# Kernel tuning notes

Measured on AMD Instinct MI355X. Metric: run time of the kernel, lower is better.

The kernel has to match this reference:

```python
import jax, jax.numpy as jnp
import numpy as np

N = 40000      # nodes
E = 400000     # edges
G = 64         # graphs in batch
IN = 128       # input feature dim
D = 64         # num_hidden (per-head out dim)
H = 4          # heads per layer
C = 10         # num_classes
SLOPE = 0.2    # leaky_relu negative slope


def setup_inputs() -> dict:
    key = jax.random.key(0)
    ks = jax.random.split(key, 16)

    def p(k, shape, fan):
        return jax.random.normal(k, shape, jnp.float32) * (1.0 / np.sqrt(fan))

    x = jax.random.normal(ks[0], (N, IN), jnp.float32)
    src = jax.random.randint(ks[1], (E,), 0, N, dtype=jnp.int32)
    dst = jax.random.randint(ks[2], (E,), 0, N, dtype=jnp.int32)
    graph_id = jnp.sort(jax.random.randint(ks[3], (N,), 0, G, dtype=jnp.int32))

    W0 = p(ks[4], (IN, H * D), IN)
    al0 = p(ks[5], (H, D), D)
    ar0 = p(ks[6], (H, D), D)
    W1 = p(ks[7], (H * D, H * D), H * D)
    al1 = p(ks[8], (H, D), D)
    ar1 = p(ks[9], (H, D), D)
    W2 = p(ks[10], (H * D, H * D), H * D)
    al2 = p(ks[11], (H, D), D)
    ar2 = p(ks[12], (H, D), D)
    Wc = p(ks[13], (D, C), D)
    bc = jnp.zeros((C,), jnp.float32)
    return dict(x=x, src=src, dst=dst, graph_id=graph_id,
                W0=W0, al0=al0, ar0=ar0, W1=W1, al1=al1, ar1=ar1,
                W2=W2, al2=al2, ar2=ar2, Wc=Wc, bc=bc)


def gat_layer(h, W, al, ar, src, dst, residual, activate):
    # DGL GATConv (no bias): project, per-edge attention, edge-softmax, aggregate.
    n = h.shape[0]
    Hh, Dd = al.shape
    feat = (h @ W).reshape(n, Hh, Dd)                       # [N,H,D]
    el = jnp.einsum('nhd,hd->nh', feat, al)                 # [N,H]
    er = jnp.einsum('nhd,hd->nh', feat, ar)                 # [N,H]
    e = jax.nn.leaky_relu(el[src] + er[dst], SLOPE)         # [E,H]
    # numerically stable edge softmax over incoming edges of each dst node
    m = jax.ops.segment_max(e, dst, num_segments=n)
    m = jnp.where(jnp.isfinite(m), m, 0.0)                  # isolated nodes -> -inf
    ee = jnp.exp(e - m[dst])                                # [E,H]
    denom = jax.ops.segment_sum(ee, dst, num_segments=n)
    alpha = ee / jnp.maximum(denom[dst], 1e-9)              # [E,H]
    msg = feat[src] * alpha[..., None]                      # [E,H,D]
    out = jax.ops.segment_sum(msg, dst, num_segments=n)     # [N,H,D]
    if residual:  # identity residual (in == H*D)
        out = out + h.reshape(n, Hh, Dd)
    if activate:
        out = jax.nn.elu(out)
    return out


def reference(x, src, dst, graph_id, W0, al0, ar0, W1, al1, ar1,
              W2, al2, ar2, Wc, bc):
    h = gat_layer(x, W0, al0, ar0, src, dst, False, True).reshape(N, H * D)
    h = gat_layer(h, W1, al1, ar1, src, dst, True, True).reshape(N, H * D)
    h = gat_layer(h, W2, al2, ar2, src, dst, True, False).mean(axis=1)  # [N,D]
    # mean_nodes readout over batched graphs
    cnt = jax.ops.segment_sum(jnp.ones((N,), jnp.float32), graph_id, num_segments=G)
    hg = jax.ops.segment_sum(h, graph_id, num_segments=G) / jnp.maximum(cnt, 1.0)[:, None]
    return hg @ Wc + bc                                     # [G,C]
```

## Files before the change

kernel.cpp:

```cpp
#include <hip/hip_runtime.h>
#include <hip/hip_bf16.h>
#include <math.h>

#define N_NODES 40000
#define N_EDGES 400000
#define N_GRAPH 64
#define IN_DIM 128
#define HD 256
#define NCLS 10
#define SLOPE 0.2f

typedef __hip_bfloat16 bf16;
typedef __attribute__((ext_vector_type(8))) short short8;
typedef __attribute__((ext_vector_type(4))) float floatx4;

__device__ __forceinline__ float b2f(bf16 x){ return __bfloat162float(x); }
__device__ __forceinline__ bf16  f2b(float x){ return __float2bfloat16(x); }

__device__ __forceinline__ floatx4 unpack4(uint2 u){
  floatx4 f;
  f[0] = __uint_as_float(u.x << 16);
  f[1] = __uint_as_float(u.x & 0xffff0000u);
  f[2] = __uint_as_float(u.y << 16);
  f[3] = __uint_as_float(u.y & 0xffff0000u);
  return f;
}

__device__ __forceinline__ int wave_incl_scan(int x, int lane){
  #pragma unroll
  for (int m=1;m<64;m<<=1){
    int v = __shfl_up(x, m);
    if (lane >= m) x += v;
  }
  return x;
}

__global__ __launch_bounds__(256) void prep_kernel(const float* __restrict__ W0, ushort* __restrict__ Wt0,
                                                   const float* __restrict__ W1, ushort* __restrict__ Wt1,
                                                   const float* __restrict__ W2, ushort* __restrict__ Wt2,
                                                   int* __restrict__ cnt, float* __restrict__ gacc)
{
  int b = blockIdx.x, t = threadIdx.x;
  if (b < 640){
    const float* W; ushort* Wt; int e0, n_el;
    if (b < 128){ W = W0; Wt = Wt0; e0 = b*256; n_el = IN_DIM*HD; }
    else if (b < 384){ W = W1; Wt = Wt1; e0 = (b-128)*256; n_el = HD*HD; }
    else { W = W2; Wt = Wt2; e0 = (b-384)*256; n_el = HD*HD; }
    int e = e0 + t;
    if (e < n_el){
      int k = e >> 8, n = e & 255;
      int idx = (((k>>6)*256 + n)<<6) + (k & 63);
      Wt[idx] = __bfloat16_as_ushort(f2b(W[e]));
    }
  } else if (b < 797){
    int i = (b-640)*256 + t;
    if (i < N_NODES) cnt[i] = 0;
  } else {
    #pragma unroll
    for (int k=0;k<16;++k) gacc[t*16 + k] = 0.f;
  }
}

__global__ __launch_bounds__(256) void hist_kernel(const int* __restrict__ dst, int* __restrict__ cnt){
  int i = blockIdx.x*256 + threadIdx.x;
  if (i < N_EDGES) atomicAdd(&cnt[dst[i]], 1);
}

__global__ __launch_bounds__(1024) void csr_scan_kernel(const int* __restrict__ cnt,
                                                        int* __restrict__ rs, int* __restrict__ cur){
  int t = threadIdx.x, b = blockIdx.x;
  int w = t>>6, l = t&63;
  int pre = 0;
  for (int i = t; i < b*1024; i += 1024) pre += cnt[i];
  #pragma unroll
  for (int m=32;m;m>>=1) pre += __shfl_down(pre, m);
  __shared__ int pw[16];
  if (l == 0) pw[w] = pre;
  __syncthreads();
  __shared__ int boff_s;
  if (t == 0){
    int s = 0;
    #pragma unroll
    for (int i=0;i<16;i++) s += pw[i];
    boff_s = s;
  }
  int idx = b*1024 + t;
  int c = (idx < N_NODES) ? cnt[idx] : 0;
  int wi = wave_incl_scan(c, l);
  __shared__ int ws[16];
  __shared__ int wexcl[16];
  if (l==63) ws[w] = wi;
  __syncthreads();
  if (t < 16){
    int x = ws[t];
    #pragma unroll
    for (int m=1;m<16;m<<=1){
      int v = __shfl_up(x, m);
      if (t >= m) x += v;
    }
    wexcl[t] = x - ws[t];
  }
  __syncthreads();
  if (idx < N_NODES){
    int p = boff_s + wexcl[w] + wi - c;
    rs[idx] = p; cur[idx] = p;
  }
  if (b == 39 && t == 0) rs[N_NODES] = N_EDGES;
}

__global__ __launch_bounds__(256) void scatter_kernel(const int* __restrict__ src, const int* __restrict__ dst,
                                                      int* __restrict__ cur, int* __restrict__ csrc){
  int i = blockIdx.x*256 + threadIdx.x;
  if (i < N_EDGES){
    int p = atomicAdd(&cur[dst[i]], 1);
    csrc[p] = src[i];
  }
}

template<int K, int AF32>
__global__ __launch_bounds__(256) void gemm_kernel(const void* __restrict__ A, const ushort* __restrict__ Wt,
                                                   bf16* __restrict__ C,
                                                   const float* __restrict__ al, const float* __restrict__ ar,
                                                   float* __restrict__ el, float* __restrict__ er)
{
  __shared__ __align__(16) short As[64][72];
  int t = threadIdx.x;
  int lane = t & 63, w = t >> 6;
  int quad = lane >> 4, l15 = lane & 15;
  int bm = blockIdx.x;
  floatx4 acc[4][4] = {};
  int srow = t >> 3, scol = (t & 7) << 3;

  for (int kc = 0; kc < K/64; ++kc){
    __syncthreads();
    #pragma unroll
    for (int i=0;i<2;++i){
      int row = srow + 32*i;
      short8 v;
      if (AF32){
        const float* Af = (const float*)A;
        const float* p = Af + (size_t)(bm*64 + row)*K + kc*64 + scol;
        float4 u0 = *(const float4*)p;
        float4 u1 = *(const float4*)(p + 4);
        v[0]=(short)__bfloat16_as_ushort(f2b(u0.x)); v[1]=(short)__bfloat16_as_ushort(f2b(u0.y));
        v[2]=(short)__bfloat16_as_ushort(f2b(u0.z)); v[3]=(short)__bfloat16_as_ushort(f2b(u0.w));
        v[4]=(short)__bfloat16_as_ushort(f2b(u1.x)); v[5]=(short)__bfloat16_as_ushort(f2b(u1.y));
        v[6]=(short)__bfloat16_as_ushort(f2b(u1.z)); v[7]=(short)__bfloat16_as_ushort(f2b(u1.w));
      } else {
        const ushort* Au = (const ushort*)A;
        v = *(const short8*)(Au + (size_t)(bm*64 + row)*K + kc*64 + scol);
      }
      *(short8*)&As[row][scol] = v;
    }
    __syncthreads();
    #pragma unroll
    for (int j=0;j<2;++j){
      short8 af[4], bfr[4];
      #pragma unroll
      for (int mt=0;mt<4;++mt) af[mt] = *(const short8*)&As[16*mt + l15][8*quad + 32*j];
      #pragma unroll
      for (int ct=0;ct<4;++ct){
        int n = w*64 + 16*ct + l15;
        bfr[ct] = *(const short8*)(Wt + ((size_t)(kc*256 + n)<<6) + 8*quad + 32*j);
      }
      #pragma unroll
      for (int mt=0;mt<4;++mt)
        #pragma unroll
        for (int ct=0;ct<4;++ct)
          acc[mt][ct] = __builtin_amdgcn_mfma_f32_16x16x32_bf16(af[mt], bfr[ct], acc[mt][ct], 0, 0, 0);
    }
  }

  #pragma unroll
  for (int mt=0;mt<4;++mt)
    #pragma unroll
    for (int ct=0;ct<4;++ct)
      #pragma unroll
      for (int r=0;r<4;++r){
        int row = bm*64 + 16*mt + 4*quad + r;
        C[(size_t)row*HD + w*64 + 16*ct + l15] = f2b(acc[mt][ct][r]);
      }

  float alv[4], arv[4];
  #pragma unroll
  for (int ct=0;ct<4;++ct){ alv[ct] = al[w*64 + 16*ct + l15]; arv[ct] = ar[w*64 + 16*ct + l15]; }
  #pragma unroll
  for (int mt=0;mt<4;++mt)
    #pragma unroll
    for (int r=0;r<4;++r){
      float pe = 0.f, pr_ = 0.f;
      #pragma unroll
      for (int ct=0;ct<4;++ct){ float v = acc[mt][ct][r]; pe += v*alv[ct]; pr_ += v*arv[ct]; }
      #pragma unroll
      for (int m=1;m<16;m<<=1){ pe += __shfl_xor(pe, m); pr_ += __shfl_xor(pr_, m); }
      if (l15 == 0){
        int row = bm*64 + 16*mt + 4*quad + r;
        el[row*4 + w] = pe;
        er[row*4 + w] = pr_;
      }
    }
}

__global__ __launch_bounds__(256) void agg_kernel(const bf16* __restrict__ feat,
                                                  const float* __restrict__ el, const float* __restrict__ er,
                                                  const int* __restrict__ rs, const int* __restrict__ csrc,
                                                  bf16* __restrict__ h_io,
                                                  int residual, int activate)
{
  int t = threadIdx.x;
  int w = t >> 6, l = t & 63;
  int n = blockIdx.x*4 + w;
  int h = l >> 4;
  float er_h = er[n*4 + h];
  int j0 = rs[n], j1 = rs[n+1];
  const uint2* fp = (const uint2*)feat;
  uint2* hp = (uint2*)h_io;

  floatx4 res = {0,0,0,0};
  if (residual) res = unpack4(hp[(size_t)n*64 + l]);

  floatx4 a0={0,0,0,0}, a1={0,0,0,0}, a2={0,0,0,0}, a3={0,0,0,0};
  float d0=0.f, d1=0.f, d2=0.f, d3=0.f;

  for (int base = j0; base < j1; base += 64){
    int m = j1 - base; if (m > 64) m = 64;
    int eidx = csrc[base + (l < m ? l : m-1)];
    int jj = 0;
    for (; jj+3 < m; jj += 4){
      int s0 = __shfl(eidx, jj),   s1 = __shfl(eidx, jj+1);
      int s2 = __shfl(eidx, jj+2), s3 = __shfl(eidx, jj+3);
      float e0 = el[s0*4+h] + er_h;
      float e1 = el[s1*4+h] + er_h;
      float e2 = el[s2*4+h] + er_h;
      float e3 = el[s3*4+h] + er_h;
      e0 = (e0 > 0.f) ? e0 : SLOPE*e0;
      e1 = (e1 > 0.f) ? e1 : SLOPE*e1;
      e2 = (e2 > 0.f) ? e2 : SLOPE*e2;
      e3 = (e3 > 0.f) ? e3 : SLOPE*e3;
      float ee0 = __expf(e0), ee1 = __expf(e1), ee2 = __expf(e2), ee3 = __expf(e3);
      floatx4 f0 = unpack4(fp[(size_t)s0*64 + l]);
      floatx4 f1 = unpack4(fp[(size_t)s1*64 + l]);
      floatx4 f2 = unpack4(fp[(size_t)s2*64 + l]);
      floatx4 f3 = unpack4(fp[(size_t)s3*64 + l]);
      d0 += ee0; d1 += ee1; d2 += ee2; d3 += ee3;
      #pragma unroll
      for (int k=0;k<4;++k){
        a0[k] += ee0*f0[k]; a1[k] += ee1*f1[k];
        a2[k] += ee2*f2[k]; a3[k] += ee3*f3[k];
      }
    }
    for (; jj < m; ++jj){
      int s0 = __shfl(eidx, jj);
      float e0 = el[s0*4+h] + er_h;
      e0 = (e0 > 0.f) ? e0 : SLOPE*e0;
      float ee0 = __expf(e0);
      floatx4 f0 = unpack4(fp[(size_t)s0*64 + l]);
      d0 += ee0;
      #pragma unroll
      for (int k=0;k<4;++k) a0[k] += ee0*f0[k];
    }
  }
  float den = fmaxf((d0+d1)+(d2+d3), 1e-9f);
  ushort4 o;
  #pragma unroll
  for (int k=0;k<4;++k){
    float v = ((a0[k]+a1[k])+(a2[k]+a3[k])) / den + res[k];
    if (activate) v = (v > 0.f) ? v : expm1f(v);
    ((ushort*)&o)[k] = __bfloat16_as_ushort(f2b(v));
  }
  *(ushort4*)&hp[(size_t)n*64 + l] = o;
}

__global__ __launch_bounds__(256) void readout_kernel(const bf16* __restrict__ h2, const int* __restrict__ gid,
                                                      float* __restrict__ gacc)
{
  int t = threadIdx.x;
  int w = t >> 6, l = t & 63;
  int nbase = blockIdx.x*64 + w*16;
  const uint2* hp = (const uint2*)h2;
  floatx4 run = {0,0,0,0};
  int curg = gid[nbase];
  for (int i=0;i<16;++i){
    int n = nbase + i;
    int g = gid[n];
    floatx4 v = unpack4(hp[(size_t)n*64 + l]);
    #pragma unroll
    for (int k=0;k<4;++k){ v[k] += __shfl_xor(v[k], 16); v[k] += __shfl_xor(v[k], 32); v[k] *= 0.25f; }
    if (g != curg){
      if (l < 16){
        #pragma unroll
        for (int k=0;k<4;++k) atomicAdd(&gacc[curg*64 + 4*l + k], run[k]);
      }
      run = (floatx4){0,0,0,0}; curg = g;
    }
    if (l < 16){
      #pragma unroll
      for (int k=0;k<4;++k) run[k] += v[k];
    }
  }
  if (l < 16){
    #pragma unroll
    for (int k=0;k<4;++k) atomicAdd(&gacc[curg*64 + 4*l + k], run[k]);
  }
}

__global__ __launch_bounds__(64) void classifier_kernel(const float* __restrict__ gacc, const int* __restrict__ gid,
                                                        const float* __restrict__ Wc, const float* __restrict__ bc,
                                                        float* __restrict__ out)
{
  int g = blockIdx.x, d = threadIdx.x;
  __shared__ float hg[64];
  __shared__ int cnt_s;
  if (d == 0){
    int lo = 0, hi = N_NODES;
    while (lo < hi){ int mid = (lo+hi)>>1; if (gid[mid] < g) lo = mid+1; else hi = mid; }
    int start = lo;
    hi = N_NODES;
    while (lo < hi){ int mid = (lo+hi)>>1; if (gid[mid] <= g) lo = mid+1; else hi = mid; }
    cnt_s = lo - start;
  }
  hg[d] = gacc[g*64+d];
  __syncthreads();
  float inv = 1.0f / fmaxf((float)cnt_s, 1.0f);
  if (d < NCLS){
    float s = 0.f;
    #pragma unroll
    for (int k=0;k<64;k++) s += hg[k] * Wc[k*NCLS + d];
    out[g*NCLS + d] = bc[d] + s * inv;
  }
}

__global__ __launch_bounds__(64) void diag_kernel(float* __restrict__ out, float v){
  int i = blockIdx.x*64 + threadIdx.x;
  if (i < N_GRAPH*NCLS) out[i] = v;
}

#define WS_NEEDED 54589216ull

extern "C" void kernel_launch(void* const* d_in, const int* in_sizes, int n_in,
                              void* d_out, int out_size, void* d_ws, size_t ws_size,
                              hipStream_t stream)
{
  (void)out_size;
  float* out = (float*)d_out;

  if (ws_size < WS_NEEDED){
    diag_kernel<<<10, 64, 0, stream>>>(out, (float)(ws_size >> 20));
    return;
  }
  static const int sz_dict[15] = {5120000,400000,400000,40000,32768,256,256,65536,256,256,65536,256,256,640,10};
  bool okd = (n_in >= 15);
  if (okd) for (int i=0;i<15;i++) if (in_sizes[i] != sz_dict[i]) { okd = false; break; }
  if (!okd){ diag_kernel<<<10, 64, 0, stream>>>(out, 3.0f); return; }

  const float* x  = (const float*)d_in[0];
  const int* src  = (const int*)d_in[1];
  const int* dst  = (const int*)d_in[2];
  const int* gid  = (const int*)d_in[3];
  const float* W0 = (const float*)d_in[4];
  const float* al0= (const float*)d_in[5];
  const float* ar0= (const float*)d_in[6];
  const float* W1 = (const float*)d_in[7];
  const float* al1= (const float*)d_in[8];
  const float* ar1= (const float*)d_in[9];
  const float* W2 = (const float*)d_in[10];
  const float* al2= (const float*)d_in[11];
  const float* ar2= (const float*)d_in[12];
  const float* Wc = (const float*)d_in[13];
  const float* bc = (const float*)d_in[14];

  char* ws = (char*)d_ws;
  int*    rs   = (int*)   (ws + 256);
  int*    csrc = (int*)   (ws + 160512);
  float*  el   = (float*) (ws + 1760512);
  float*  er   = (float*) (ws + 2400512);
  int*    cnt  = (int*)   (ws + 1760512);
  int*    cur  = (int*)   (ws + 2400512);
  bf16*   H    = (bf16*)  (ws + 3040512);
  bf16*   feat = (bf16*)  (ws + 23520512);
  float*  gacc = (float*) (ws + 44000512);
  ushort* Wt0  = (ushort*)(ws + 54257152);
  ushort* Wt1  = (ushort*)(ws + 54322688);
  ushort* Wt2  = (ushort*)(ws + 54453760);

  prep_kernel<<<798, 256, 0, stream>>>(W0, Wt0, W1, Wt1, W2, Wt2, cnt, gacc);

  const int eb = (N_EDGES + 255)/256;
  hist_kernel    <<<eb, 256, 0, stream>>>(dst, cnt);
  csr_scan_kernel<<<40, 1024, 0, stream>>>(cnt, rs, cur);
  scatter_kernel <<<eb, 256, 0, stream>>>(src, dst, cur, csrc);

  gemm_kernel<IN_DIM,1><<<625, 256, 0, stream>>>(x, Wt0, feat, al0, ar0, el, er);
  agg_kernel<<<N_NODES/4, 256, 0, stream>>>(feat, el, er, rs, csrc, H, 0, 1);
  gemm_kernel<HD,0><<<625, 256, 0, stream>>>(H, Wt1, feat, al1, ar1, el, er);
  agg_kernel<<<N_NODES/4, 256, 0, stream>>>(feat, el, er, rs, csrc, H, 1, 1);
  gemm_kernel<HD,0><<<625, 256, 0, stream>>>(H, Wt2, feat, al2, ar2, el, er);
  agg_kernel<<<N_NODES/4, 256, 0, stream>>>(feat, el, er, rs, csrc, H, 1, 0);
  readout_kernel   <<<625, 256, 0, stream>>>(H, gid, gacc);
  classifier_kernel<<<N_GRAPH, 64, 0, stream>>>(gacc, gid, Wc, bc, out);
}
```

Baseline: 342.9 us.

## Fuse graph-build kernels into neighbors, last-block classifier, deeper agg unroll

Folds the histogram into the weight-prep kernel, replacing the zeroing blocks with a memset. Runs the CSR scatter inside the first GEMM launch as extra blocks. Merges the classifier into the readout kernel using a last-block-done counter. The aggregation inner loop now batches eight gathered neighbors, so more loads are in flight before they are used. These changes cut kernel launches and their gaps, and add latency hiding in the gather. The cost is more register pressure in agg and a serial tail in the last readout block.

```diff
diff --git a/kernel.cpp b/kernel.cpp
--- a/kernel.cpp
+++ b/kernel.cpp
@@ -9,6 +9,7 @@
 #define HD 256
 #define NCLS 10
 #define SLOPE 0.2f
+#define SCAT_B 1563
 
 typedef __hip_bfloat16 bf16;
 typedef __attribute__((ext_vector_type(8))) short short8;
@@ -35,10 +36,11 @@
   return x;
 }
 
-__global__ __launch_bounds__(256) void prep_kernel(const float* __restrict__ W0, ushort* __restrict__ Wt0,
-                                                   const float* __restrict__ W1, ushort* __restrict__ Wt1,
-                                                   const float* __restrict__ W2, ushort* __restrict__ Wt2,
-                                                   int* __restrict__ cnt, float* __restrict__ gacc)
+__global__ __launch_bounds__(256) void prep_hist_kernel(const float* __restrict__ W0, ushort* __restrict__ Wt0,
+                                                        const float* __restrict__ W1, ushort* __restrict__ Wt1,
+                                                        const float* __restrict__ W2, ushort* __restrict__ Wt2,
+                                                        const int* __restrict__ dst, int* __restrict__ cnt,
+                                                        float* __restrict__ gacc, int* __restrict__ gdone)
 {
   int b = blockIdx.x, t = threadIdx.x;
   if (b < 640){
@@ -52,18 +54,14 @@
       int idx = (((k>>6)*256 + n)<<6) + (k & 63);
       Wt[idx] = __bfloat16_as_ushort(f2b(W[e]));
     }
-  } else if (b < 797){
+  } else if (b < 2203){
     int i = (b-640)*256 + t;
-    if (i < N_NODES) cnt[i] = 0;
+    if (i < N_EDGES) atomicAdd(&cnt[dst[i]], 1);
   } else {
     #pragma unroll
     for (int k=0;k<16;++k) gacc[t*16 + k] = 0.f;
-  }
-}
-
-__global__ __launch_bounds__(256) void hist_kernel(const int* __restrict__ dst, int* __restrict__ cnt){
-  int i = blockIdx.x*256 + threadIdx.x;
-  if (i < N_EDGES) atomicAdd(&cnt[dst[i]], 1);
+    if (t == 0) *gdone = 0;
+  }
 }
 
 __global__ __launch_bounds__(1024) void csr_scan_kernel(const int* __restrict__ cnt,
@@ -108,26 +106,16 @@
   if (b == 39 && t == 0) rs[N_NODES] = N_EDGES;
 }
 
-__global__ __launch_bounds__(256) void scatter_kernel(const int* __restrict__ src, const int* __restrict__ dst,
-                                                      int* __restrict__ cur, int* __restrict__ csrc){
-  int i = blockIdx.x*256 + threadIdx.x;
-  if (i < N_EDGES){
-    int p = atomicAdd(&cur[dst[i]], 1);
-    csrc[p] = src[i];
-  }
-}
-
 template<int K, int AF32>
-__global__ __launch_bounds__(256) void gemm_kernel(const void* __restrict__ A, const ushort* __restrict__ Wt,
-                                                   bf16* __restrict__ C,
-                                                   const float* __restrict__ al, const float* __restrict__ ar,
-                                                   float* __restrict__ el, float* __restrict__ er)
+__device__ __forceinline__ void gemm_body(int bm, const void* __restrict__ A, const ushort* __restrict__ Wt,
+                                          bf16* __restrict__ C,
+                                          const float* __restrict__ al, const float* __restrict__ ar,
+                                          float* __restrict__ el, float* __restrict__ er)
 {
   __shared__ __align__(16) short As[64][72];
   int t = threadIdx.x;
   int lane = t & 63, w = t >> 6;
   int quad = lane >> 4, l15 = lane & 15;
-  int bm = blockIdx.x;
   floatx4 acc[4][4] = {};
   int srow = t >> 3, scol = (t & 7) << 3;
 
@@ -201,6 +189,32 @@
     }
 }
 
+__global__ __launch_bounds__(256) void gemm_kernel(const void* __restrict__ A, const ushort* __restrict__ Wt,
+                                                   bf16* __restrict__ C,
+                                                   const float* __restrict__ al, const float* __restrict__ ar,
+                                                   float* __restrict__ el, float* __restrict__ er)
+{
+  gemm_body<HD,0>(blockIdx.x, A, Wt, C, al, ar, el, er);
+}
+
+__global__ __launch_bounds__(256) void gemm0_scatter_kernel(const void* __restrict__ A, const ushort* __restrict__ Wt,
+                                                            bf16* __restrict__ C,
+                                                            const float* __restrict__ al, const float* __restrict__ ar,
+                                                            float* __restrict__ el, float* __restrict__ er,
+                                                            const int* __restrict__ src, const int* __restrict__ dst,
+                                                            int* __restrict__ cur, int* __restrict__ csrc)
+{
+  if (blockIdx.x < SCAT_B){
+    int i = blockIdx.x*256 + threadIdx.x;
+    if (i < N_EDGES){
+      int p = atomicAdd(&cur[dst[i]], 1);
+      csrc[p] = src[i];
+    }
+    return;
+  }
+  gemm_body<IN_DIM,1>(blockIdx.x - SCAT_B, A, Wt, C, al, ar, el, er);
+}
+
 __global__ __launch_bounds__(256) void agg_kernel(const bf16* __restrict__ feat,
                                                   const float* __restrict__ el, const float* __restrict__ er,
                                                   const int* __restrict__ rs, const int* __restrict__ csrc,
@@ -226,27 +240,24 @@
     int m = j1 - base; if (m > 64) m = 64;
     int eidx = csrc[base + (l < m ? l : m-1)];
     int jj = 0;
-    for (; jj+3 < m; jj += 4){
-      int s0 = __shfl(eidx, jj),   s1 = __shfl(eidx, jj+1);
-      int s2 = __shfl(eidx, jj+2), s3 = __shfl(eidx, jj+3);
-      float e0 = el[s0*4+h] + er_h;
-      float e1 = el[s1*4+h] + er_h;
-      float e2 = el[s2*4+h] + er_h;
-      float e3 = el[s3*4+h] + er_h;
-      e0 = (e0 > 0.f) ? e0 : SLOPE*e0;
-      e1 = (e1 > 0.f) ? e1 : SLOPE*e1;
-      e2 = (e2 > 0.f) ? e2 : SLOPE*e2;
-      e3 = (e3 > 0.f) ? e3 : SLOPE*e3;
-      float ee0 = __expf(e0), ee1 = __expf(e1), ee2 = __expf(e2), ee3 = __expf(e3);
-      floatx4 f0 = unpack4(fp[(size_t)s0*64 + l]);
-      floatx4 f1 = unpack4(fp[(size_t)s1*64 + l]);
-      floatx4 f2 = unpack4(fp[(size_t)s2*64 + l]);
-      floatx4 f3 = unpack4(fp[(size_t)s3*64 + l]);
-      d0 += ee0; d1 += ee1; d2 += ee2; d3 += ee3;
-      #pragma unroll
-      for (int k=0;k<4;++k){
-        a0[k] += ee0*f0[k]; a1[k] += ee1*f1[k];
-        a2[k] += ee2*f2[k]; a3[k] += ee3*f3[k];
+    for (; jj+7 < m; jj += 8){
+      int   sA[8]; float eA[8]; uint2 uA[8];
+      #pragma unroll
+      for (int q=0;q<8;++q) sA[q] = __shfl(eidx, jj+q);
+      #pragma unroll
+      for (int q=0;q<8;++q) eA[q] = el[sA[q]*4+h];
+      #pragma unroll
+      for (int q=0;q<8;++q) uA[q] = fp[(size_t)sA[q]*64 + l];
+      #pragma unroll
+      for (int q=0;q<8;++q){
+        float e = eA[q] + er_h;
+        e = (e > 0.f) ? e : SLOPE*e;
+        float ee = __expf(e);
+        floatx4 f = unpack4(uA[q]);
+        if ((q&3)==0){ d0 += ee; for (int k=0;k<4;++k) a0[k] += ee*f[k]; }
+        else if ((q&3)==1){ d1 += ee; for (int k=0;k<4;++k) a1[k] += ee*f[k]; }
+        else if ((q&3)==2){ d2 += ee; for (int k=0;k<4;++k) a2[k] += ee*f[k]; }
+        else { d3 += ee; for (int k=0;k<4;++k) a3[k] += ee*f[k]; }
       }
     }
     for (; jj < m; ++jj){
@@ -271,8 +282,10 @@
   *(ushort4*)&hp[(size_t)n*64 + l] = o;
 }
 
-__global__ __launch_bounds__(256) void readout_kernel(const bf16* __restrict__ h2, const int* __restrict__ gid,
-                                                      float* __restrict__ gacc)
+__global__ __launch_bounds__(256) void readout_cls_kernel(const bf16* __restrict__ h2, const int* __restrict__ gid,
+                                                          float* __restrict__ gacc, int* __restrict__ gdone,
+                                                          const float* __restrict__ Wc, const float* __restrict__ bc,
+                                                          float* __restrict__ out)
 {
   int t = threadIdx.x;
   int w = t >> 6, l = t & 63;
@@ -302,31 +315,34 @@
     #pragma unroll
     for (int k=0;k<4;++k) atomicAdd(&gacc[curg*64 + 4*l + k], run[k]);
   }
-}
-
-__global__ __launch_bounds__(64) void classifier_kernel(const float* __restrict__ gacc, const int* __restrict__ gid,
-                                                        const float* __restrict__ Wc, const float* __restrict__ bc,
-                                                        float* __restrict__ out)
-{
-  int g = blockIdx.x, d = threadIdx.x;
-  __shared__ float hg[64];
-  __shared__ int cnt_s;
-  if (d == 0){
-    int lo = 0, hi = N_NODES;
-    while (lo < hi){ int mid = (lo+hi)>>1; if (gid[mid] < g) lo = mid+1; else hi = mid; }
-    int start = lo;
-    hi = N_NODES;
-    while (lo < hi){ int mid = (lo+hi)>>1; if (gid[mid] <= g) lo = mid+1; else hi = mid; }
-    cnt_s = lo - start;
-  }
-  hg[d] = gacc[g*64+d];
+
+  __threadfence();
   __syncthreads();
-  float inv = 1.0f / fmaxf((float)cnt_s, 1.0f);
-  if (d < NCLS){
-    float s = 0.f;
-    #pragma unroll
-    for (int k=0;k<64;k++) s += hg[k] * Wc[k*NCLS + d];
-    out[g*NCLS + d] = bc[d] + s * inv;
+  __shared__ int last_s;
+  if (t == 0) last_s = (atomicAdd(gdone, 1) == 624) ? 1 : 0;
+  __syncthreads();
+  if (!last_s) return;
+
+  for (int i=0;i<16;++i){
+    int g = w*16 + i;
+    float hgv = atomicAdd(&gacc[g*64 + l], 0.0f);
+    int cntv = 0;
+    if (l == 0){
+      int lo = 0, hi = N_NODES;
+      while (lo < hi){ int mid = (lo+hi)>>1; if (gid[mid] < g) lo = mid+1; else hi = mid; }
+      int st = lo; hi = N_NODES;
+      while (lo < hi){ int mid = (lo+hi)>>1; if (gid[mid] <= g) lo = mid+1; else hi = mid; }
+      cntv = lo - st;
+    }
+    cntv = __shfl(cntv, 0);
+    float inv = 1.0f / fmaxf((float)cntv, 1.0f);
+    #pragma unroll
+    for (int d=0; d<NCLS; ++d){
+      float p = hgv * Wc[l*NCLS + d];
+      #pragma unroll
+      for (int m2=1;m2<64;m2<<=1) p += __shfl_xor(p, m2);
+      if (l == 0) out[g*NCLS + d] = bc[d] + p * inv;
+    }
   }
 }
 
@@ -379,23 +395,23 @@
   bf16*   H    = (bf16*)  (ws + 3040512);
   bf16*   feat = (bf16*)  (ws + 23520512);
   float*  gacc = (float*) (ws + 44000512);
+  int*    gdone= (int*)   (ws + 44016896);
   ushort* Wt0  = (ushort*)(ws + 54257152);
   ushort* Wt1  = (ushort*)(ws + 54322688);
   ushort* Wt2  = (ushort*)(ws + 54453760);
 
-  prep_kernel<<<798, 256, 0, stream>>>(W0, Wt0, W1, Wt1, W2, Wt2, cnt, gacc);
-
-  const int eb = (N_EDGES + 255)/256;
-  hist_kernel    <<<eb, 256, 0, stream>>>(dst, cnt);
-  csr_scan_kernel<<<40, 1024, 0, stream>>>(cnt, rs, cur);
-  scatter_kernel <<<eb, 256, 0, stream>>>(src, dst, cur, csrc);
-
-  gemm_kernel<IN_DIM,1><<<625, 256, 0, stream>>>(x, Wt0, feat, al0, ar0, el, er);
+  int* cur_safe = (int*)(ws + 44017152);
+
+  hipMemsetAsync(cnt, 0, N_NODES*sizeof(int), stream);
+  prep_hist_kernel<<<2204, 256, 0, stream>>>(W0, Wt0, W1, Wt1, W2, Wt2, dst, cnt, gacc, gdone);
+  csr_scan_kernel<<<40, 1024, 0, stream>>>(cnt, rs, cur_safe);
+
+  gemm0_scatter_kernel<<<SCAT_B + 625, 256, 0, stream>>>(x, Wt0, feat, al0, ar0, el, er,
+                                                         src, dst, cur_safe, csrc);
   agg_kernel<<<N_NODES/4, 256, 0, stream>>>(feat, el, er, rs, csrc, H, 0, 1);
-  gemm_kernel<HD,0><<<625, 256, 0, stream>>>(H, Wt1, feat, al1, ar1, el, er);
+  gemm_kernel<<<625, 256, 0, stream>>>(H, Wt1, feat, al1, ar1, el, er);
   agg_kernel<<<N_NODES/4, 256, 0, stream>>>(feat, el, er, rs, csrc, H, 1, 1);
-  gemm_kernel<HD,0><<<625, 256, 0, stream>>>(H, Wt2, feat, al2, ar2, el, er);
+  gemm_kernel<<<625, 256, 0, stream>>>(H, Wt2, feat, al2, ar2, el, er);
   agg_kernel<<<N_NODES/4, 256, 0, stream>>>(feat, el, er, rs, csrc, H, 1, 0);
-  readout_kernel   <<<625, 256, 0, stream>>>(H, gid, gacc);
-  classifier_kernel<<<N_GRAPH, 64, 0, stream>>>(gacc, gid, Wc, bc, out);
-}
+  readout_cls_kernel<<<625, 256, 0, stream>>>(H, gid, gacc, gdone, Wc, bc, out);
+}
```

After: 493.5 us. 43.9% more time.
